# Performance work log

Hardware: AMD Instinct MI355X
Metric: run time of the kernel (lower is better)

Reference implementation:

```python
import jax, jax.numpy as jnp
import numpy as np

S = 64        # num_states
ODIM = 8      # padded neighbor-feature width
H = 256       # HIDDEN_DIM
A = 16        # num_actions
B = 16384     # batch (dtpt)
IDIM = S + ODIM
NEG_SLOPE = 0.01  # nn.LeakyReLU default
EPS = 1e-5        # nn.LayerNorm default


def setup_inputs() -> dict:
    key = jax.random.key(0)
    ks = jax.random.split(key, 8)
    x = jax.random.normal(ks[0], (B, S), jnp.float32)
    # per-state neighbor indices into x's feature dim, padded to ODIM with a mask
    o_idx = jax.random.randint(ks[1], (S, ODIM), 0, S)
    o_len = jax.random.randint(ks[2], (S,), 1, ODIM + 1)
    o_mask = jnp.arange(ODIM)[None, :] < o_len[:, None]  # [S, ODIM] bool

    def lin(k, fin, fout):
        bound = 1.0 / np.sqrt(fin)
        kw, kb = jax.random.split(k)
        W = jax.random.uniform(kw, (S, fin, fout), jnp.float32, -bound, bound)
        b = jax.random.uniform(kb, (S, fout), jnp.float32, -bound, bound)
        return W, b

    W1, b1 = lin(ks[3], IDIM, H)
    W2, b2 = lin(ks[4], H, H)
    Wp, bp = lin(ks[5], H, A)
    g1 = jnp.ones((S, H), jnp.float32); be1 = jnp.zeros((S, H), jnp.float32)
    g2 = jnp.ones((S, H), jnp.float32); be2 = jnp.zeros((S, H), jnp.float32)
    return dict(x=x, o_idx=o_idx, o_mask=o_mask, W1=W1, b1=b1, g1=g1, be1=be1,
                W2=W2, b2=b2, g2=g2, be2=be2, Wp=Wp, bp=bp)


def _layer_norm(h, g, b):
    # h: [B, S, H], per-state affine params g,b: [S, H]
    mu = jnp.mean(h, axis=-1, keepdims=True)
    var = jnp.mean((h - mu) ** 2, axis=-1, keepdims=True)
    return (h - mu) * jax.lax.rsqrt(var + EPS) * g[None] + b[None]


def reference(x, o_idx, o_mask, W1, b1, g1, be1, W2, b2, g2, be2, Wp, bp):
    # irregular gather: for each state s take x[:, o_nbr_index[s]], zero-pad to ODIM
    o = jnp.where(o_mask[None, :, :], x[:, o_idx], jnp.float32(0))  # [B, S, ODIM]
    one_hot = jnp.broadcast_to(jnp.eye(S, dtype=x.dtype)[None], (x.shape[0], S, S))
    inp = jnp.concatenate([one_hot, o], axis=-1)  # [B, S, IDIM]

    h = jnp.einsum('bsi,sih->bsh', inp, W1) + b1[None]
    h = _layer_norm(jax.nn.leaky_relu(h, NEG_SLOPE), g1, be1)
    h = jnp.einsum('bsh,shk->bsk', h, W2) + b2[None]
    h = _layer_norm(jax.nn.leaky_relu(h, NEG_SLOPE), g2, be2)
    pi_logit = jnp.einsum('bsh,sha->bsa', h, Wp) + bp[None]  # [B, S, A]
    lg_sm = jax.nn.log_softmax(pi_logit, axis=-1)
    return pi_logit, lg_sm
```

## Files before the change

kernel.cpp:

```cpp
#include <hip/hip_runtime.h>

#define LNEPS 1e-5f

typedef __attribute__((ext_vector_type(8)))  short          bf16x8;
typedef __attribute__((ext_vector_type(8)))  unsigned short u16x8;
typedef __attribute__((ext_vector_type(4)))  float          f32x4;
typedef __attribute__((ext_vector_type(16))) float          f32x16;
typedef __attribute__((ext_vector_type(4)))  unsigned int   u32x4;

#define MFMA32(a, b, c) __builtin_amdgcn_mfma_f32_32x32x16_bf16((a), (b), (c), 0, 0, 0)

#define WS_W2G  0
#define WS_A1   8388608
#define WS_WPG  8912896
#define WS_UC2  10027008
#define WS_MIDX 10092544
#define WS_XG   10094592

union U8 { bf16x8 v; unsigned u[4]; };

__device__ __forceinline__ unsigned short f2bf(float v) {
  union { float f; unsigned u; } a; a.f = v;
  unsigned r = a.u + 0x7fffu + ((a.u >> 16) & 1u);
  return (unsigned short)(r >> 16);
}
__device__ __forceinline__ unsigned cvtpk(float lo, float hi) {
  unsigned r;
  asm("v_cvt_pk_bf16_f32 %0, %1, %2" : "=v"(r) : "v"(lo), "v"(hi));
  return r;
}
__device__ __forceinline__ void swap2(unsigned& a, unsigned& b) {
  asm volatile("v_permlane32_swap_b32 %0, %1" : "+v"(a), "+v"(b));
}

__global__ void prep_midx_k(const int* __restrict__ oidx,
                            const unsigned* __restrict__ mask32,
                            int* __restrict__ midx) {
  __shared__ int fgt1, ffl;
  const int t = threadIdx.x;
  if (t == 0) { fgt1 = 0; ffl = 0; }
  __syncthreads();
  if (t < 128) {
    unsigned wv = mask32[t];
    if (wv == 0x3f800000u) atomicOr(&ffl, 1);
    else if (wv > 1u)      atomicOr(&fgt1, 1);
  }
  __syncthreads();
  const int mode = ffl ? 2 : (fgt1 ? 1 : 0);
  int mv;
  if (mode == 2)      mv = (((const float*)mask32)[t] != 0.0f) ? 1 : 0;
  else if (mode == 1) mv = (int)((const unsigned char*)mask32)[t];
  else                mv = ((const int*)mask32)[t];
  midx[t] = (mv != 0) ? oidx[t] : -1;
}

__global__ __launch_bounds__(256) void prep_xg_k(
    const float* __restrict__ x, const int* __restrict__ midx,
    u32x4* __restrict__ xg) {
  const int g = blockIdx.x * 256 + threadIdx.x;
  const int s = g >> 14, row = g & 16383;
  const float* xr = x + (size_t)row * 64;
  const int* mi = midx + s * 8;
  u32x4 w;
#pragma unroll
  for (int p = 0; p < 4; ++p) {
    const int m0 = mi[2 * p], m1 = mi[2 * p + 1];
    const float a = m0 < 0 ? 0.f : xr[m0];
    const float b = m1 < 0 ? 0.f : xr[m1];
    w[p] = (unsigned)f2bf(a) | ((unsigned)f2bf(b) << 16);
  }
  xg[g] = w;
}

__global__ __launch_bounds__(256) void prep_w2g_k(
    const float* __restrict__ W2, const float* __restrict__ g1,
    unsigned short* __restrict__ w2g) {
  const int tid = blockIdx.x * 256 + threadIdx.x;
  const int l = tid & 63;
  const int t = (tid >> 6) & 15;
  const int i = (tid >> 10) & 7;
  const int s = tid >> 13;
  const int n = i * 32 + (l & 31);
  const int h = l >> 5;
  const float* w = W2 + (size_t)s * 65536;
  const float* g = g1 + s * 256;
  u16x8 v;
#pragma unroll
  for (int j = 0; j < 8; ++j) {
    const int k = t * 16 + h * 8 + j;
    v[j] = f2bf(w[k * 256 + n] * g[k]);
  }
  ((u16x8*)w2g)[tid] = v;
}

__global__ __launch_bounds__(256) void prep_uc2_k(
    const float* __restrict__ W2, const float* __restrict__ g1,
    const float* __restrict__ be1, const float* __restrict__ b2,
    unsigned* __restrict__ uc2) {
  const int tid = blockIdx.x * 256 + threadIdx.x;
  const int s = tid >> 8, n = tid & 255;
  const float* w = W2 + (size_t)s * 65536 + n;
  const float* g = g1 + s * 256;
  const float* be = be1 + s * 256;
  float u = 0.f, c = 0.f;
#pragma unroll 8
  for (int k = 0; k < 256; ++k) {
    const float wk = w[k * 256];
    u = fmaf(wk, g[k], u);
    c = fmaf(wk, be[k], c);
  }
  c += b2[tid];
  uc2[tid] = (unsigned)f2bf(u) | ((unsigned)f2bf(c) << 16);
}

__global__ __launch_bounds__(256) void prep_a1_k(
    const float* __restrict__ W1, const float* __restrict__ b1,
    unsigned short* __restrict__ a1b) {
  const int tid = blockIdx.x * 256 + threadIdx.x;
  const int l = tid & 63;
  const int i = (tid >> 6) & 7;
  const int s = tid >> 9;
  const int n = i * 32 + (l & 31);
  const float* w = W1 + (size_t)s * 72 * 256;
  u16x8 v;
#pragma unroll
  for (int j = 0; j < 8; ++j) v[j] = 0;
  if (l < 32) {
#pragma unroll
    for (int j = 0; j < 8; ++j) v[j] = f2bf(w[(64 + j) * 256 + n]);
  } else {
    v[0] = f2bf(w[s * 256 + n] + b1[s * 256 + n]);
  }
  ((u16x8*)a1b)[tid] = v;
}

__global__ __launch_bounds__(256) void prep_wpg_k(
    const float* __restrict__ Wp, const float* __restrict__ g2,
    const float* __restrict__ be2, const float* __restrict__ bp,
    unsigned short* __restrict__ wpg) {
  const int tid = blockIdx.x * 256 + threadIdx.x;
  const int l = tid & 63;
  const int r = tid >> 6;
  const int t = r % 17;
  const int s = r / 17;
  const int a = l & 31;
  const int h = l >> 5;
  u16x8 v;
#pragma unroll
  for (int j = 0; j < 8; ++j) v[j] = 0;
  if (t < 16) {
    if (a < 16) {
      const float* w = Wp + (size_t)s * 4096;
      const float* g = g2 + s * 256;
#pragma unroll
      for (int j = 0; j < 8; ++j) {
        const int k = t * 16 + h * 8 + j;
        v[j] = f2bf(w[k * 16 + a] * g[k]);
      }
    }
  } else if (h == 0 && a < 16) {
    const float* w = Wp + (size_t)s * 4096;
    float up = 0.f, cp = 0.f;
#pragma unroll 8
    for (int k = 0; k < 256; ++k) {
      const float wk = w[k * 16 + a];
      up = fmaf(wk, g2[s * 256 + k], up);
      cp = fmaf(wk, be2[s * 256 + k], cp);
    }
    cp += bp[s * 16 + a];
    v[0] = f2bf(up); v[1] = f2bf(cp);
  }
  ((u16x8*)wpg)[tid] = v;
}

__device__ __forceinline__ void pack_tile(const f32x16& a,
                                          unsigned* f0, unsigned* f1) {
  unsigned w0 = cvtpk(a[0], a[1]),   w1 = cvtpk(a[2], a[3]);
  unsigned w2 = cvtpk(a[4], a[5]),   w3 = cvtpk(a[6], a[7]);
  unsigned w4 = cvtpk(a[8], a[9]),   w5 = cvtpk(a[10], a[11]);
  unsigned w6 = cvtpk(a[12], a[13]), w7 = cvtpk(a[14], a[15]);
  swap2(w0, w2); swap2(w1, w3); swap2(w4, w6); swap2(w5, w7);
  f0[0] = w0; f0[1] = w1; f0[2] = w2; f0[3] = w3;
  f1[0] = w4; f1[1] = w5; f1[2] = w6; f1[3] = w7;
}

__global__ __launch_bounds__(512, 2) void actor_main(
    const u32x4* __restrict__ xg,
    const unsigned short* __restrict__ w2g, const unsigned* __restrict__ uc2,
    const unsigned short* __restrict__ a1b, const unsigned short* __restrict__ wpg,
    float* __restrict__ out) {
  extern __shared__ char lds[];
  const int tid = threadIdx.x;
  const int wv = tid >> 6;
  const int l = tid & 63;
  const int bl = l & 31;
  const int h = l >> 5;
  const int s = blockIdx.x >> 2;
  const int rowstart = (blockIdx.x & 3) << 12;

  {
    const u32x4* src = (const u32x4*)(w2g + (size_t)s * 65536);
    u32x4* dst = (u32x4*)lds;
#pragma unroll
    for (int i = 0; i < 16; ++i) dst[i * 512 + tid] = src[i * 512 + tid];
  }

  unsigned aext[8];
#pragma unroll
  for (int i = 0; i < 8; ++i) {
    const unsigned t = uc2[(s * 8 + i) * 32 + bl];
    aext[i] = h ? 0u : t;
  }
  const bf16x8* A1 = ((const bf16x8*)a1b) + (size_t)(s * 8) * 64 + l;
  const bf16x8* A3 = ((const bf16x8*)wpg) + (size_t)(s * 17) * 64 + l;
  const char* ldsl = lds + (l << 4);
  const u32x4* XG = xg + ((size_t)s << 14);

  const int rbase = rowstart + wv * 32 + bl;

  u32x4 gcur = XG[rbase];

  __syncthreads();

  for (int it = 0; it < 16; ++it) {
    const int row = rbase + it * 256;

    U8 B1;
    B1.u[0] = h ? 0x00003F80u : gcur[0];
    B1.u[1] = h ? 0u : gcur[1];
    B1.u[2] = h ? 0u : gcur[2];
    B1.u[3] = h ? 0u : gcur[3];

    gcur = XG[rbase + ((it + 1) & 15) * 256];

    float s0 = 0.f, s1 = 0.f, q0 = 0.f, q1 = 0.f;
    f32x16 acc2[8];
    bf16x8 a1n = A1[64];
    bf16x8 Afc[8];
#pragma unroll
    for (int j = 0; j < 8; ++j)
      Afc[j] = *(const bf16x8*)(ldsl + ((j * 16 + 0) << 10));

    f32x16 accP;
    { f32x16 z = {}; accP = MFMA32(A1[0], B1.v, z); }

#pragma unroll
    for (int i = 0; i < 8; ++i) {
      f32x16 yv;
#pragma unroll
      for (int r = 0; r < 16; ++r) {
        float v = accP[r];
        v = fmaxf(v, 0.01f * v);
        yv[r] = v;
        if (r & 1) { s1 += v; q1 = fmaf(v, v, q1); }
        else       { s0 += v; q0 = fmaf(v, v, q0); }
      }
      U8 Bf0, Bf1;
      pack_tile(yv, Bf0.u, Bf1.u);

      if (i < 7) {
        f32x16 z = {};
        accP = MFMA32(a1n, B1.v, z);
        if (i < 6) a1n = A1[(i + 2) * 64];
      }

#pragma unroll
      for (int j = 0; j < 8; ++j) {
        if (i == 0) { f32x16 zz = {}; acc2[j] = MFMA32(Afc[j], Bf0.v, zz); }
        else        { acc2[j] = MFMA32(Afc[j], Bf0.v, acc2[j]); }
      }
      bf16x8 Afn[8];
#pragma unroll
      for (int j = 0; j < 8; ++j)
        Afn[j] = *(const bf16x8*)(ldsl + ((j * 16 + 2 * i + 1) << 10));
#pragma unroll
      for (int j = 0; j < 8; ++j) acc2[j] = MFMA32(Afn[j], Bf1.v, acc2[j]);
      if (i < 7) {
#pragma unroll
        for (int j = 0; j < 8; ++j)
          Afc[j] = *(const bf16x8*)(ldsl + ((j * 16 + 2 * i + 2) << 10));
      }
    }

    float sum = s0 + s1, ssq = q0 + q1;
    sum += __shfl_xor(sum, 32, 64);
    ssq += __shfl_xor(ssq, 32, 64);
    const float m1 = sum * 0.00390625f;
    const float var1 = fmaf(ssq, 0.00390625f, -m1 * m1) + LNEPS;
    const float rho1 = rsqrtf(var1);
    const float std1 = var1 * rho1;
    const unsigned be2w = cvtpk(-m1, std1);
    bf16x8 p0 = A3[0], p1 = A3[64];
    {
      U8 Bx; Bx.u[0] = h ? 0u : be2w; Bx.u[1] = 0; Bx.u[2] = 0; Bx.u[3] = 0;
#pragma unroll
      for (int i = 0; i < 8; ++i) {
        U8 Ax; Ax.u[0] = aext[i]; Ax.u[1] = 0; Ax.u[2] = 0; Ax.u[3] = 0;
        acc2[i] = MFMA32(Ax.v, Bx.v, acc2[i]);
      }
    }

    f32x16 a3a = {}, a3b = {};
    s0 = s1 = q0 = q1 = 0.f;
#pragma unroll
    for (int i = 0; i < 8; ++i) {
      bf16x8 n0, n1;
      if (i < 7) { n0 = A3[(2 * i + 2) * 64]; n1 = A3[(2 * i + 3) * 64]; }
      else       { n0 = A3[16 * 64]; n1 = p1; }
      f32x16 yv;
#pragma unroll
      for (int r = 0; r < 16; ++r) {
        float v = acc2[i][r];
        v = fmaxf(v, 0.01f * v);
        yv[r] = v;
        if (r & 1) { s1 += v; q1 = fmaf(v, v, q1); }
        else       { s0 += v; q0 = fmaf(v, v, q0); }
      }
      U8 Bf0, Bf1;
      pack_tile(yv, Bf0.u, Bf1.u);
      a3a = MFMA32(p0, Bf0.v, a3a);
      a3b = MFMA32(p1, Bf1.v, a3b);
      p0 = n0; p1 = n1;
    }
    float sum2 = s0 + s1, ssq2 = q0 + q1;
    sum2 += __shfl_xor(sum2, 32, 64);
    ssq2 += __shfl_xor(ssq2, 32, 64);
    const float mp = sum2 * 0.00390625f;
    const float qp = ssq2 * 0.00390625f;
    const float var2 = rho1 * rho1 * fmaf(-mp, mp, qp) + LNEPS;
    const float rho2 = rsqrtf(var2);
    const float sigma = rho1 * rho2;
    const float inv = var2 * rho2 * std1;
    const unsigned be3w = cvtpk(-mp, inv);
    {
      U8 Bx; Bx.u[0] = h ? 0u : be3w; Bx.u[1] = 0; Bx.u[2] = 0; Bx.u[3] = 0;
      a3a = MFMA32(p0, Bx.v, a3a);
    }

    float lg[8];
#pragma unroll
    for (int r = 0; r < 8; ++r) lg[r] = sigma * (a3a[r] + a3b[r]);
    float mx = fmaxf(fmaxf(fmaxf(lg[0], lg[1]), fmaxf(lg[2], lg[3])),
                     fmaxf(fmaxf(lg[4], lg[5]), fmaxf(lg[6], lg[7])));
    mx = fmaxf(mx, __shfl_xor(mx, 32, 64));
    float es = 0.f;
#pragma unroll
    for (int r = 0; r < 8; ++r) es += __expf(lg[r] - mx);
    es += __shfl_xor(es, 32, 64);
    const float lse = mx + __logf(es);

    const size_t ob = (((size_t)row << 6) + s) * 16 + (h << 2);
    f32x4 v0 = {lg[0], lg[1], lg[2], lg[3]};
    f32x4 v1 = {lg[4], lg[5], lg[6], lg[7]};
    *(f32x4*)(out + ob) = v0;
    *(f32x4*)(out + ob + 8) = v1;
    f32x4 w0 = {lg[0] - lse, lg[1] - lse, lg[2] - lse, lg[3] - lse};
    f32x4 w1 = {lg[4] - lse, lg[5] - lse, lg[6] - lse, lg[7] - lse};
    *(f32x4*)(out + 16777216 + ob) = w0;
    *(f32x4*)(out + 16777216 + ob + 8) = w1;
  }
}

extern "C" void kernel_launch(void* const* d_in, const int* in_sizes, int n_in,
                              void* d_out, int out_size, void* d_ws, size_t ws_size,
                              hipStream_t stream) {
  const float* x    = (const float*)d_in[0];
  const int*   oidx = (const int*)d_in[1];
  const unsigned* omask = (const unsigned*)d_in[2];
  const float* W1 = (const float*)d_in[3];
  const float* b1 = (const float*)d_in[4];
  const float* g1 = (const float*)d_in[5];
  const float* be1 = (const float*)d_in[6];
  const float* W2 = (const float*)d_in[7];
  const float* b2 = (const float*)d_in[8];
  const float* g2 = (const float*)d_in[9];
  const float* be2 = (const float*)d_in[10];
  const float* Wp = (const float*)d_in[11];
  const float* bp = (const float*)d_in[12];
  float* out = (float*)d_out;

  char* ws = (char*)d_ws;
  unsigned short* wsW2G = (unsigned short*)(ws + WS_W2G);
  unsigned short* wsA1  = (unsigned short*)(ws + WS_A1);
  unsigned short* wsWPG = (unsigned short*)(ws + WS_WPG);
  unsigned*       wsUC2 = (unsigned*)(ws + WS_UC2);
  int*            wsMIDX = (int*)(ws + WS_MIDX);
  u32x4*          wsXG   = (u32x4*)(ws + WS_XG);

  prep_midx_k<<<1, 512, 0, stream>>>(oidx, omask, wsMIDX);
  prep_xg_k<<<4096, 256, 0, stream>>>(x, wsMIDX, wsXG);
  prep_w2g_k<<<2048, 256, 0, stream>>>(W2, g1, wsW2G);
  prep_uc2_k<<<64, 256, 0, stream>>>(W2, g1, be1, b2, wsUC2);
  prep_a1_k<<<128, 256, 0, stream>>>(W1, b1, wsA1);
  prep_wpg_k<<<272, 256, 0, stream>>>(Wp, g2, be2, bp, wsWPG);

  hipFuncSetAttribute((const void*)actor_main,
                      hipFuncAttributeMaxDynamicSharedMemorySize, 131072);
  actor_main<<<256, 512, 131072, stream>>>(
      wsXG, wsW2G, wsUC2, wsA1, wsWPG, out);
}
```

Measured before the change: 288.9 us.

## Restructure layer-2 GEMM to output-tile-major order and interleave block-to-state mapping

The second-layer matmul no longer keeps eight 16-float accumulators live across the whole K loop. It first packs all layer-1 activations into bf16 fragments (64 registers), then computes each 32-wide output tile to completion with a single accumulator. Each finished tile is fed directly into the LN2 and policy-head stage, which cuts register pressure and may avoid spills at the 512-thread, 2-block launch bound. The block index mapping also changes so that consecutive blocks handle different states rather than the same state. This alters L2 reuse of weights and inputs, and the K-accumulation chain per tile becomes serial, which could reduce MFMA overlap.

```diff
diff --git a/kernel.cpp b/kernel.cpp
--- a/kernel.cpp
+++ b/kernel.cpp
@@ -195,8 +195,8 @@
   const int l = tid & 63;
   const int bl = l & 31;
   const int h = l >> 5;
-  const int s = blockIdx.x >> 2;
-  const int rowstart = (blockIdx.x & 3) << 12;
+  const int s = blockIdx.x & 63;
+  const int rowstart = (blockIdx.x >> 6) << 12;
 
   {
     const u32x4* src = (const u32x4*)(w2g + (size_t)s * 65536);
@@ -224,6 +224,11 @@
 
   for (int it = 0; it < 16; ++it) {
     const int row = rbase + it * 256;
+
+    bf16x8 bufA[8];
+#pragma unroll
+    for (int t = 0; t < 8; ++t)
+      bufA[t] = *(const bf16x8*)(ldsl + (t << 10));
 
     U8 B1;
     B1.u[0] = h ? 0x00003F80u : gcur[0];
@@ -234,16 +239,10 @@
     gcur = XG[rbase + ((it + 1) & 15) * 256];
 
     float s0 = 0.f, s1 = 0.f, q0 = 0.f, q1 = 0.f;
-    f32x16 acc2[8];
+    unsigned yf[16][4];
     bf16x8 a1n = A1[64];
-    bf16x8 Afc[8];
-#pragma unroll
-    for (int j = 0; j < 8; ++j)
-      Afc[j] = *(const bf16x8*)(ldsl + ((j * 16 + 0) << 10));
-
     f32x16 accP;
     { f32x16 z = {}; accP = MFMA32(A1[0], B1.v, z); }
-
 #pragma unroll
     for (int i = 0; i < 8; ++i) {
       f32x16 yv;
@@ -255,33 +254,13 @@
         if (r & 1) { s1 += v; q1 = fmaf(v, v, q1); }
         else       { s0 += v; q0 = fmaf(v, v, q0); }
       }
-      U8 Bf0, Bf1;
-      pack_tile(yv, Bf0.u, Bf1.u);
-
       if (i < 7) {
         f32x16 z = {};
         accP = MFMA32(a1n, B1.v, z);
         if (i < 6) a1n = A1[(i + 2) * 64];
       }
-
-#pragma unroll
-      for (int j = 0; j < 8; ++j) {
-        if (i == 0) { f32x16 zz = {}; acc2[j] = MFMA32(Afc[j], Bf0.v, zz); }
-        else        { acc2[j] = MFMA32(Afc[j], Bf0.v, acc2[j]); }
-      }
-      bf16x8 Afn[8];
-#pragma unroll
-      for (int j = 0; j < 8; ++j)
-        Afn[j] = *(const bf16x8*)(ldsl + ((j * 16 + 2 * i + 1) << 10));
-#pragma unroll
-      for (int j = 0; j < 8; ++j) acc2[j] = MFMA32(Afn[j], Bf1.v, acc2[j]);
-      if (i < 7) {
-#pragma unroll
-        for (int j = 0; j < 8; ++j)
-          Afc[j] = *(const bf16x8*)(ldsl + ((j * 16 + 2 * i + 2) << 10));
-      }
+      pack_tile(yv, yf[2 * i], yf[2 * i + 1]);
     }
-
     float sum = s0 + s1, ssq = q0 + q1;
     sum += __shfl_xor(sum, 32, 64);
     ssq += __shfl_xor(ssq, 32, 64);
@@ -290,27 +269,49 @@
     const float rho1 = rsqrtf(var1);
     const float std1 = var1 * rho1;
     const unsigned be2w = cvtpk(-m1, std1);
-    bf16x8 p0 = A3[0], p1 = A3[64];
-    {
-      U8 Bx; Bx.u[0] = h ? 0u : be2w; Bx.u[1] = 0; Bx.u[2] = 0; Bx.u[3] = 0;
-#pragma unroll
-      for (int i = 0; i < 8; ++i) {
-        U8 Ax; Ax.u[0] = aext[i]; Ax.u[1] = 0; Ax.u[2] = 0; Ax.u[3] = 0;
-        acc2[i] = MFMA32(Ax.v, Bx.v, acc2[i]);
-      }
-    }
+    U8 Bx2; Bx2.u[0] = h ? 0u : be2w; Bx2.u[1] = 0; Bx2.u[2] = 0; Bx2.u[3] = 0;
 
     f32x16 a3a = {}, a3b = {};
     s0 = s1 = q0 = q1 = 0.f;
-#pragma unroll
-    for (int i = 0; i < 8; ++i) {
+    bf16x8 p0 = A3[0], p1 = A3[64];
+#pragma unroll
+    for (int j = 0; j < 8; ++j) {
+      const char* tb = ldsl + (j << 14);
+      bf16x8 bufB[8];
+#pragma unroll
+      for (int t = 0; t < 8; ++t)
+        bufB[t] = *(const bf16x8*)(tb + ((t + 8) << 10));
+      f32x16 acc;
+#pragma unroll
+      for (int t = 0; t < 8; ++t) {
+        U8 Bf; Bf.u[0] = yf[t][0]; Bf.u[1] = yf[t][1];
+        Bf.u[2] = yf[t][2]; Bf.u[3] = yf[t][3];
+        if (t == 0) { f32x16 z = {}; acc = MFMA32(bufA[0], Bf.v, z); }
+        else        { acc = MFMA32(bufA[t], Bf.v, acc); }
+      }
+      if (j < 7) {
+        const char* tn = ldsl + ((j + 1) << 14);
+#pragma unroll
+        for (int t = 0; t < 8; ++t)
+          bufA[t] = *(const bf16x8*)(tn + (t << 10));
+      }
+#pragma unroll
+      for (int t = 0; t < 8; ++t) {
+        U8 Bf; Bf.u[0] = yf[t + 8][0]; Bf.u[1] = yf[t + 8][1];
+        Bf.u[2] = yf[t + 8][2]; Bf.u[3] = yf[t + 8][3];
+        acc = MFMA32(bufB[t], Bf.v, acc);
+      }
+      {
+        U8 Ax; Ax.u[0] = aext[j]; Ax.u[1] = 0; Ax.u[2] = 0; Ax.u[3] = 0;
+        acc = MFMA32(Ax.v, Bx2.v, acc);
+      }
       bf16x8 n0, n1;
-      if (i < 7) { n0 = A3[(2 * i + 2) * 64]; n1 = A3[(2 * i + 3) * 64]; }
+      if (j < 7) { n0 = A3[(2 * j + 2) * 64]; n1 = A3[(2 * j + 3) * 64]; }
       else       { n0 = A3[16 * 64]; n1 = p1; }
       f32x16 yv;
 #pragma unroll
       for (int r = 0; r < 16; ++r) {
-        float v = acc2[i][r];
+        float v = acc[r];
         v = fmaxf(v, 0.01f * v);
         yv[r] = v;
         if (r & 1) { s1 += v; q1 = fmaf(v, v, q1); }
```

Result: slower. 315.0 us (+9.0%).
